# Performance work log

Measured on AMD Instinct MI355X. Metric: run time of the kernel, lower is better.

## Reference

```python
import jax, jax.numpy as jnp
import numpy as np

D = 1024
H = 16
HD = D // H
SCALE = HD ** -0.5
EPS = 1e-5

def _ln(x, g, b):
    m = jnp.mean(x, axis=-1, keepdims=True)
    v = jnp.mean((x - m) ** 2, axis=-1, keepdims=True)
    return (x - m) / jnp.sqrt(v + EPS) * g + b

def setup_inputs() -> dict:
    key = jax.random.key(0)
    ks = jax.random.split(key, 16)
    B, Lq, Lk = 8, 1024, 1024
    s = 0.02
    inp = {
        "q": jax.random.normal(ks[0], (B, Lq, D), jnp.float32),
        "kv": jax.random.normal(ks[1], (B, Lk, D), jnp.float32),
        "kv_mask": jax.random.randint(ks[2], (B, Lk), 0, 2).astype(bool),
        "Wq": jax.random.normal(ks[3], (D, D), jnp.float32) * s,
        "bq": jnp.zeros((D,), jnp.float32),
        "Wk": jax.random.normal(ks[4], (D, D), jnp.float32) * s,
        "bk": jnp.zeros((D,), jnp.float32),
        "Wv": jax.random.normal(ks[5], (D, D), jnp.float32) * s,
        "bv": jnp.zeros((D,), jnp.float32),
        "Wo": jax.random.normal(ks[6], (D, D), jnp.float32) * s,
        "bo": jnp.zeros((D,), jnp.float32),
        "ln1_g": jnp.ones((D,), jnp.float32),
        "ln1_b": jnp.zeros((D,), jnp.float32),
        "W1": jax.random.normal(ks[7], (D, 4 * D), jnp.float32) * s,
        "b1": jnp.zeros((4 * D,), jnp.float32),
        "W2": jax.random.normal(ks[8], (4 * D, D), jnp.float32) * s,
        "b2": jnp.zeros((D,), jnp.float32),
        "ln2_g": jnp.ones((D,), jnp.float32),
        "ln2_b": jnp.zeros((D,), jnp.float32),
    }
    return inp

def reference(q, kv, kv_mask, Wq, bq, Wk, bk, Wv, bv, Wo, bo, ln1_g, ln1_b, W1, b1, W2, b2, ln2_g, ln2_b):
    B, Lq, _ = q.shape
    Lk = kv.shape[1]
    # projections -> [B, H, L, HD]
    qp = (q @ Wq + bq).reshape(B, Lq, H, HD).transpose(0, 2, 1, 3)
    kp = (kv @ Wk + bk).reshape(B, Lk, H, HD).transpose(0, 2, 1, 3)
    vp = (kv @ Wv + bv).reshape(B, Lk, H, HD).transpose(0, 2, 1, 3)
    scores = jnp.einsum('bhqd,bhkd->bhqk', qp, kp) * SCALE
    # mask: True = pad; if a row is all-pad, un-mask the last key position
    all_pad = jnp.all(kv_mask, axis=1)  # [B]
    mask = kv_mask.at[:, -1].set(jnp.where(all_pad, False, kv_mask[:, -1]))
    scores = jnp.where(mask[:, None, None, :], jnp.float32(-10000.0), scores)
    attn = jax.nn.softmax(scores, axis=-1)  # dropout is identity at eval
    out = jnp.einsum('bhqk,bhkd->bhqd', attn, vp)
    out = out.transpose(0, 2, 1, 3).reshape(B, Lq, D)
    out = out @ Wo + bo
    x = _ln(q + out, ln1_g, ln1_b)
    x2 = jax.nn.relu(x @ W1 + b1) @ W2 + b2
    return _ln(x + x2, ln2_g, ln2_b)
```

## Files before the change

kernel.cpp:

```cpp
#include <hip/hip_runtime.h>

typedef __bf16 bf16_t;
typedef bf16_t bf16x8 __attribute__((ext_vector_type(8)));
typedef bf16_t bf16x4 __attribute__((ext_vector_type(4)));
typedef float f32x4 __attribute__((ext_vector_type(4)));
typedef unsigned int u32;

typedef __attribute__((address_space(1))) unsigned as1_u32;
typedef __attribute__((address_space(3))) unsigned as3_u32;

#define LOG2E 1.4426950408889634f
#define QSCALE (0.125f * LOG2E)
#define MASK2 (-10000.0f * LOG2E)

__device__ __forceinline__ void gload16(const void* g, void* l) {
  __builtin_amdgcn_global_load_lds((as1_u32*)(void*)g, (as3_u32*)l, 16, 0, 0);
}

__global__ void cvt_qkv(const float* __restrict__ q, const float* __restrict__ kv,
                        bf16_t* __restrict__ qb, bf16_t* __restrict__ kvb) {
  long i = ((long)blockIdx.x * 256 + threadIdx.x) * 8;
  const float* src; bf16_t* dst;
  if (i < 8388608) { src = q + i; dst = qb + i; }
  else { src = kv + (i - 8388608); dst = kvb + (i - 8388608); }
  const float4 a = *(const float4*)src;
  const float4 b = *(const float4*)(src + 4);
  bf16x8 o;
  o[0] = (bf16_t)a.x; o[1] = (bf16_t)a.y; o[2] = (bf16_t)a.z; o[3] = (bf16_t)a.w;
  o[4] = (bf16_t)b.x; o[5] = (bf16_t)b.y; o[6] = (bf16_t)b.z; o[7] = (bf16_t)b.w;
  *(bf16x8*)dst = o;
}

__global__ void prep_mask(const unsigned char* __restrict__ mraw,
                          float* __restrict__ maskf) {
  __shared__ int sred[256];
  const int t = threadIdx.x, b = blockIdx.x;
  int f = 0;
  for (int i = t; i < 2048; i += 256) {
    u32 v = ((const u32*)mraw)[i];
    if (v & 0xFFFFFF00u) f = 1;
  }
  sred[t] = f; __syncthreads();
  for (int s = 128; s; s >>= 1) { if (t < s) sred[t] |= sred[t + s]; __syncthreads(); }
  const int isByte = sred[0];
  __syncthreads();

  int vals[4]; int allpad = 1;
#pragma unroll
  for (int i = 0; i < 4; i++) {
    int k = t * 4 + i;
    int mv = isByte ? (int)mraw[b * 1024 + k] : ((const int*)mraw)[b * 1024 + k];
    vals[i] = (mv != 0);
    allpad &= vals[i];
  }
  sred[t] = allpad; __syncthreads();
  for (int s = 128; s; s >>= 1) { if (t < s) sred[t] &= sred[t + s]; __syncthreads(); }
  const int ap = sred[0];
#pragma unroll
  for (int i = 0; i < 4; i++) {
    int k = t * 4 + i;
    int m = vals[i];
    if (ap && k == 1023) m = 0;
    maskf[b * 1024 + k] = m ? MASK2 : 0.0f;
  }
}

struct TP { const float* s; bf16_t* d; int K; int N; };
struct TP6 { TP t[6]; };
__global__ void transpose_all(TP6 args) {
  __shared__ float tile[64][65];
  int bid = blockIdx.x, z, tx, ty;
  if (bid < 1024)      { z = bid >> 8;  int r = bid & 255;  tx = r & 15; ty = r >> 4; }
  else if (bid < 2048) { z = 4;         int r = bid - 1024; tx = r & 63; ty = r >> 6; }
  else                 { z = 5;         int r = bid - 2048; tx = r & 15; ty = r >> 4; }
  const TP a = args.t[z];
  const int t = threadIdx.x;
  const int n0 = tx * 64, k0 = ty * 64;
#pragma unroll
  for (int i = 0; i < 16; i++) {
    int e = i * 256 + t; int r = e >> 6, c = e & 63;
    tile[r][c] = a.s[(size_t)(k0 + r) * a.N + n0 + c];
  }
  __syncthreads();
#pragma unroll
  for (int i = 0; i < 16; i++) {
    int e = i * 256 + t; int r = e >> 6, c = e & 63;
    a.d[(size_t)(n0 + r) * a.K + k0 + c] = (bf16_t)tile[c][r];
  }
}

template<int BM, int BN, int NT>
__global__ __launch_bounds__(NT, 2)
void gemm_bt(const bf16_t* __restrict__ A, const bf16_t* __restrict__ BT,
             const float* __restrict__ bias, bf16_t* __restrict__ C,
             int M, int N, int K, int relu, int bias_mode, float scale) {
  constexpr int WAVES = NT / 64;
  constexpr int WNC = (BN == 256) ? 4 : 2;
  constexpr int WMC = WAVES / WNC;
  constexpr int M_REP = BM / (WMC * 16);
  constexpr int N_REP = BN / (WNC * 16);
  constexpr int JA = BM * 8 / NT;
  constexpr int JB = BN * 8 / NT;

  __shared__ __align__(16) bf16_t As[2][BM * 64];
  __shared__ __align__(16) bf16_t Bs[2][BN * 64];

  const int tid = threadIdx.x;
  const int wave = tid >> 6, lane = tid & 63;
  const int quad = lane >> 4, l15 = lane & 15;
  const int gx = gridDim.x;
  const int nwg = gx * gridDim.y;
  int lin = blockIdx.y * gx + blockIdx.x;
  lin = (lin & 7) * (nwg >> 3) + (lin >> 3);
  const long bm = (long)(lin / gx) * BM, bn = (long)(lin % gx) * BN;
  const int wm = (wave / WNC) * (M_REP * 16), wn = (wave % WNC) * (N_REP * 16);

  const bf16_t* agp[JA];
  const bf16_t* bgp[JB];
#pragma unroll
  for (int j = 0; j < JA; j++) {
    int e = j * NT + tid, r = e >> 3, c = (e & 7) ^ (r & 7);
    agp[j] = A + (bm + r) * (long)K + c * 8;
  }
#pragma unroll
  for (int j = 0; j < JB; j++) {
    int e = j * NT + tid, r = e >> 3, c = (e & 7) ^ (r & 7);
    bgp[j] = BT + (bn + r) * (long)K + c * 8;
  }

  int aoff[M_REP][2], boff[N_REP][2];
#pragma unroll
  for (int mi = 0; mi < M_REP; mi++)
#pragma unroll
    for (int ks = 0; ks < 2; ks++) {
      int row = wm + mi * 16 + l15;
      aoff[mi][ks] = row * 64 + (((ks * 4 + quad) ^ (row & 7)) * 8);
    }
#pragma unroll
  for (int ni = 0; ni < N_REP; ni++)
#pragma unroll
    for (int ks = 0; ks < 2; ks++) {
      int row = wn + ni * 16 + l15;
      boff[ni][ks] = row * 64 + (((ks * 4 + quad) ^ (row & 7)) * 8);
    }

  f32x4 acc[M_REP][N_REP];
#pragma unroll
  for (int i = 0; i < M_REP; i++)
#pragma unroll
    for (int j = 0; j < N_REP; j++) acc[i][j] = (f32x4){0.f, 0.f, 0.f, 0.f};

  auto stage = [&](int kt, int s) {
#pragma unroll
    for (int j = 0; j < JA; j++)
      gload16(agp[j] + (long)kt * 64, &As[s][(j * NT + wave * 64) * 8]);
#pragma unroll
    for (int j = 0; j < JB; j++)
      gload16(bgp[j] + (long)kt * 64, &Bs[s][(j * NT + wave * 64) * 8]);
  };

  const int T = K >> 6;
  stage(0, 0);
  for (int t = 0; t < T; t++) {
    const int s = t & 1;
    if (t + 1 < T) {
      stage(t + 1, s ^ 1);
      asm volatile("s_waitcnt vmcnt(8)" ::: "memory");
    } else {
      asm volatile("s_waitcnt vmcnt(0)" ::: "memory");
    }
    __builtin_amdgcn_s_barrier();

#pragma unroll
    for (int ks = 0; ks < 2; ks++) {
      bf16x8 af[M_REP], bf[N_REP];
#pragma unroll
      for (int mi = 0; mi < M_REP; mi++) af[mi] = *(const bf16x8*)&As[s][aoff[mi][ks]];
#pragma unroll
      for (int ni = 0; ni < N_REP; ni++) bf[ni] = *(const bf16x8*)&Bs[s][boff[ni][ks]];
      __builtin_amdgcn_s_setprio(1);
#pragma unroll
      for (int mi = 0; mi < M_REP; mi++)
#pragma unroll
        for (int ni = 0; ni < N_REP; ni++)
          acc[mi][ni] = __builtin_amdgcn_mfma_f32_16x16x32_bf16(af[mi], bf[ni], acc[mi][ni], 0, 0, 0);
      __builtin_amdgcn_s_setprio(0);
    }
    asm volatile("s_waitcnt lgkmcnt(0)" ::: "memory");
    __builtin_amdgcn_s_barrier();
  }

#pragma unroll
  for (int mi = 0; mi < M_REP; mi++) {
#pragma unroll
    for (int ni = 0; ni < N_REP; ni++) {
      const long col = bn + wn + ni * 16 + l15;
      const float bc = bias_mode ? 0.f : bias[col];
#pragma unroll
      for (int r = 0; r < 4; r++) {
        const long row = bm + wm + mi * 16 + quad * 4 + r;
        const float bb = bias_mode ? bias[row] : bc;
        float v = (acc[mi][ni][r] + bb) * scale;
        if (relu) v = v > 0.f ? v : 0.f;
        C[row * N + col] = (bf16_t)v;
      }
    }
  }
}

__global__ __launch_bounds__(512, 2)
void gemm_8p(const bf16_t* __restrict__ A, const bf16_t* __restrict__ BT,
             const float* __restrict__ bias, bf16_t* __restrict__ C,
             int M, int N, int K, int relu, float scale) {
  __shared__ __align__(16) bf16_t As[2][256 * 64];
  __shared__ __align__(16) bf16_t Bs[2][256 * 64];

  const int tid = threadIdx.x;
  const int wave = tid >> 6, lane = tid & 63;
  const int quad = lane >> 4, l15 = lane & 15;
  const int gx = gridDim.x;
  const int nwg = gx * gridDim.y;
  int lin = blockIdx.y * gx + blockIdx.x;
  lin = (lin & 7) * (nwg >> 3) + (lin >> 3);
  const long bm = (long)(lin / gx) * 256, bn = (long)(lin % gx) * 256;
  const int wm = (wave >> 2) * 128, wn = (wave & 3) * 64;

  const int r_ = tid >> 3;
  const int cs_ = ((tid & 7) ^ (r_ & 7)) * 8;
  const bf16_t* ag = A + (bm + r_) * (long)K + cs_;
  const bf16_t* bg = BT + (bn + r_) * (long)K + cs_;

  int aoff[8][2], boff[4][2];
#pragma unroll
  for (int mi = 0; mi < 8; mi++)
#pragma unroll
    for (int ks = 0; ks < 2; ks++) {
      int row = wm + mi * 16 + l15;
      aoff[mi][ks] = row * 64 + (((ks * 4 + quad) ^ (row & 7)) * 8);
    }
#pragma unroll
  for (int ni = 0; ni < 4; ni++)
#pragma unroll
    for (int ks = 0; ks < 2; ks++) {
      int row = wn + ni * 16 + l15;
      boff[ni][ks] = row * 64 + (((ks * 4 + quad) ^ (row & 7)) * 8);
    }

  f32x4 acc[8][4];
#pragma unroll
  for (int i = 0; i < 8; i++)
#pragma unroll
    for (int j = 0; j < 4; j++) acc[i][j] = (f32x4){0.f, 0.f, 0.f, 0.f};

  auto stagePair = [&](int kt, int s, int j) {
    gload16(ag + (long)(j * 64) * K + (long)kt * 64, &As[s][(j * 512 + wave * 64) * 8]);
    gload16(bg + (long)(j * 64) * K + (long)kt * 64, &Bs[s][(j * 512 + wave * 64) * 8]);
  };

  const int T = K >> 6;
#pragma unroll
  for (int j = 0; j < 4; j++) stagePair(0, 0, j);

#pragma unroll 1
  for (int t = 0; t < T; t++) {
    const int s = t & 1;
    if (t + 1 < T) {
      stagePair(t + 1, s ^ 1, 0);
      asm volatile("s_waitcnt vmcnt(2)" ::: "memory");
    } else {
      asm volatile("s_waitcnt vmcnt(0)" ::: "memory");
    }
    __builtin_amdgcn_s_barrier();

    bf16x8 bf[4][2];
#pragma unroll
    for (int ni = 0; ni < 4; ni++)
#pragma unroll
      for (int ks = 0; ks < 2; ks++)
        bf[ni][ks] = *(const bf16x8*)&Bs[s][boff[ni][ks]];

#pragma unroll
    for (int p = 0; p < 4; p++) {
      bf16x8 af[2][2];
#pragma unroll
      for (int i = 0; i < 2; i++)
#pragma unroll
        for (int ks = 0; ks < 2; ks++)
          af[i][ks] = *(const bf16x8*)&As[s][aoff[p * 2 + i][ks]];
      if (p < 3 && t + 1 < T) stagePair(t + 1, s ^ 1, p + 1);
      __builtin_amdgcn_s_barrier();
      __builtin_amdgcn_s_setprio(1);
#pragma unroll
      for (int i = 0; i < 2; i++)
#pragma unroll
        for (int ni = 0; ni < 4; ni++)
#pragma unroll
          for (int ks = 0; ks < 2; ks++)
            acc[p * 2 + i][ni] = __builtin_amdgcn_mfma_f32_16x16x32_bf16(
                af[i][ks], bf[ni][ks], acc[p * 2 + i][ni], 0, 0, 0);
      __builtin_amdgcn_s_setprio(0);
      __builtin_amdgcn_s_barrier();
    }
  }

#pragma unroll
  for (int mi = 0; mi < 8; mi++) {
#pragma unroll
    for (int ni = 0; ni < 4; ni++) {
      const long col = bn + wn + ni * 16 + l15;
      const float bc = bias[col];
#pragma unroll
      for (int r = 0; r < 4; r++) {
        const long row = bm + wm + mi * 16 + quad * 4 + r;
        float v = (acc[mi][ni][r] + bc) * scale;
        if (relu) v = v > 0.f ? v : 0.f;
        C[row * N + col] = (bf16_t)v;
      }
    }
  }
}

__global__ __launch_bounds__(256, 4)
void attn(const bf16_t* __restrict__ Q, const bf16_t* __restrict__ Kp,
          const bf16_t* __restrict__ Vt, const float* __restrict__ maskf,
          bf16_t* __restrict__ AO) {
  __shared__ __align__(16) bf16_t Qs[64 * 64];
  __shared__ __align__(16) bf16_t Ks[64 * 64];
  __shared__ __align__(16) bf16_t Vts[64 * 64];
  __shared__ __align__(16) bf16_t Ps[4][16 * 64];
  __shared__ __align__(16) float msk[64];

  const int tid = threadIdx.x;
  const int wave = tid >> 6, lane = tid & 63;
  const int quad = lane >> 4, l15 = lane & 15;
  int lin = (blockIdx.z * 16 + blockIdx.y) * 16 + blockIdx.x;
  lin = (lin & 7) * 256 + (lin >> 3);
  const int q0 = (lin & 15) * 64;
  const int h = (lin >> 4) & 15;
  const int b = lin >> 8;

  const long base_q = ((long)b * 1024 + q0) * 1024 + h * 64;
  const long base_k = (long)b * 1024 * 1024 + h * 64;
  const long base_v = (long)h * 64 * 8192 + b * 1024;

  const int r0 = tid >> 3;
  const int c0 = ((tid & 7) ^ (r0 & 7)) * 8;
  const int r1 = (256 + tid) >> 3;
  const int c1 = (((256 + tid) & 7) ^ (r1 & 7)) * 8;
  const int wd0 = wave * 64 * 8;
  const int wd1 = (256 + wave * 64) * 8;

  const bf16_t* qg0 = Q + base_q + (long)r0 * 1024 + c0;
  const bf16_t* qg1 = Q + base_q + (long)r1 * 1024 + c1;
  const bf16_t* kg0 = Kp + base_k + (long)r0 * 1024 + c0;
  const bf16_t* kg1 = Kp + base_k + (long)r1 * 1024 + c1;
  const bf16_t* vg0 = Vt + base_v + (long)r0 * 8192 + c0;
  const bf16_t* vg1 = Vt + base_v + (long)r1 * 8192 + c1;
  const float* mrow = maskf + b * 1024;

  gload16(qg0, &Qs[wd0]);
  gload16(qg1, &Qs[wd1]);

  int offKV[4][2], offP[2], pwOff[4];
#pragma unroll
  for (int nt = 0; nt < 4; nt++)
#pragma unroll
    for (int ks = 0; ks < 2; ks++)
      offKV[nt][ks] = (nt * 16 + l15) * 64 + (((ks * 4 + quad) ^ (l15 & 7)) * 8);
#pragma unroll
  for (int ks = 0; ks < 2; ks++)
    offP[ks] = l15 * 64 + (((ks * 4 + quad) ^ (l15 & 7)) * 8);
#pragma unroll
  for (int nt = 0; nt < 4; nt++)
    pwOff[nt] = l15 * 64 + (((nt * 2 + (quad >> 1)) ^ (l15 & 7)) * 8) + (quad & 1) * 4;

  __syncthreads();

  bf16x8 aq[2];
#pragma unroll
  for (int ks = 0; ks < 2; ks++) {
    const int row = wave * 16 + l15;
    aq[ks] = *(const bf16x8*)&Qs[row * 64 + (((ks * 4 + quad) ^ (row & 7)) * 8)];
  }

  float l_i = 0.f;
  f32x4 o[4];
#pragma unroll
  for (int nt = 0; nt < 4; nt++) o[nt] = (f32x4){0.f, 0.f, 0.f, 0.f};

  bf16_t* Pw = &Ps[wave][0];

  for (int kt = 0; kt < 16; kt++) {
    const int k0 = kt * 64;
    __syncthreads();
    gload16(kg0 + (long)k0 * 1024, &Ks[wd0]);
    gload16(kg1 + (long)k0 * 1024, &Ks[wd1]);
    gload16(vg0 + k0, &Vts[wd0]);
    gload16(vg1 + k0, &Vts[wd1]);
    if (tid < 64) msk[tid] = mrow[k0 + tid];
    __syncthreads();

    f32x4 mv[4];
#pragma unroll
    for (int nt = 0; nt < 4; nt++)
      mv[nt] = *(const f32x4*)&msk[nt * 16 + quad * 4];

    f32x4 sc[4];
#pragma unroll
    for (int nt = 0; nt < 4; nt++) {
      f32x4 s = mv[nt];
#pragma unroll
      for (int ks = 0; ks < 2; ks++) {
        bf16x8 bk = *(const bf16x8*)&Ks[offKV[nt][ks]];
        s = __builtin_amdgcn_mfma_f32_16x16x32_bf16(bk, aq[ks], s, 0, 0, 0);
      }
      sc[nt] = s;
    }

#pragma unroll
    for (int nt = 0; nt < 4; nt++)
#pragma unroll
      for (int r = 0; r < 4; r++) {
        const float p = exp2f(sc[nt][r]);
        sc[nt][r] = p;
        l_i += p;
      }

#pragma unroll
    for (int nt = 0; nt < 4; nt++) {
      bf16x4 pv;
#pragma unroll
      for (int r = 0; r < 4; r++) pv[r] = (bf16_t)sc[nt][r];
      *(bf16x4*)&Pw[pwOff[nt]] = pv;
    }

#pragma unroll
    for (int ks = 0; ks < 2; ks++) {
      bf16x8 ap = *(const bf16x8*)&Pw[offP[ks]];
#pragma unroll
      for (int nt = 0; nt < 4; nt++) {
        bf16x8 bv = *(const bf16x8*)&Vts[offKV[nt][ks]];
        o[nt] = __builtin_amdgcn_mfma_f32_16x16x32_bf16(ap, bv, o[nt], 0, 0, 0);
      }
    }
  }

  l_i += __shfl_xor(l_i, 16);
  l_i += __shfl_xor(l_i, 32);
  float linv[4];
#pragma unroll
  for (int r = 0; r < 4; r++)
    linv[r] = 1.0f / __shfl(l_i, (quad << 4) | (quad * 4 + r));
#pragma unroll
  for (int r = 0; r < 4; r++) {
    const int row = q0 + wave * 16 + quad * 4 + r;
#pragma unroll
    for (int nt = 0; nt < 4; nt++) {
      const int col = h * 64 + nt * 16 + l15;
      AO[((long)b * 1024 + row) * 1024 + col] = (bf16_t)(o[nt][r] * linv[r]);
    }
  }
}

__global__ __launch_bounds__(256)
void ln_res1(const float* __restrict__ xa, const bf16_t* __restrict__ xb,
             const float* __restrict__ g, const float* __restrict__ bt,
             bf16_t* __restrict__ out) {
  __shared__ float sw[8];
  const int t = threadIdx.x, w = t >> 6;
  const long row = blockIdx.x;
  const float4 a = *(const float4*)(xa + row * 1024 + t * 4);
  const bf16x4 bq = *(const bf16x4*)(xb + row * 1024 + t * 4);
  float v[4] = {a.x + (float)bq[0], a.y + (float)bq[1],
                a.z + (float)bq[2], a.w + (float)bq[3]};
  float s = v[0] + v[1] + v[2] + v[3];
  float s2 = v[0]*v[0] + v[1]*v[1] + v[2]*v[2] + v[3]*v[3];
#pragma unroll
  for (int off = 1; off < 64; off <<= 1) {
    s += __shfl_xor(s, off); s2 += __shfl_xor(s2, off);
  }
  if ((t & 63) == 0) { sw[w] = s; sw[4 + w] = s2; }
  __syncthreads();
  s = sw[0] + sw[1] + sw[2] + sw[3];
  s2 = sw[4] + sw[5] + sw[6] + sw[7];
  const float mean = s * (1.f / 1024.f);
  const float var = s2 * (1.f / 1024.f) - mean * mean;
  const float rstd = rsqrtf(var + 1e-5f);
  bf16x4 o;
#pragma unroll
  for (int i = 0; i < 4; i++) {
    const int c = t * 4 + i;
    o[i] = (bf16_t)((v[i] - mean) * rstd * g[c] + bt[c]);
  }
  *(bf16x4*)(out + row * 1024 + t * 4) = o;
}

__global__ __launch_bounds__(256)
void ln_res2(const bf16_t* __restrict__ xa, const bf16_t* __restrict__ xb,
             const float* __restrict__ g, const float* __restrict__ bt,
             float* __restrict__ out) {
  __shared__ float sw[8];
  const int t = threadIdx.x, w = t >> 6;
  const long row = blockIdx.x;
  const bf16x4 aq = *(const bf16x4*)(xa + row * 1024 + t * 4);
  const bf16x4 bq = *(const bf16x4*)(xb + row * 1024 + t * 4);
  float v[4];
#pragma unroll
  for (int i = 0; i < 4; i++) v[i] = (float)aq[i] + (float)bq[i];
  float s = v[0] + v[1] + v[2] + v[3];
  float s2 = v[0]*v[0] + v[1]*v[1] + v[2]*v[2] + v[3]*v[3];
#pragma unroll
  for (int off = 1; off < 64; off <<= 1) {
    s += __shfl_xor(s, off); s2 += __shfl_xor(s2, off);
  }
  if ((t & 63) == 0) { sw[w] = s; sw[4 + w] = s2; }
  __syncthreads();
  s = sw[0] + sw[1] + sw[2] + sw[3];
  s2 = sw[4] + sw[5] + sw[6] + sw[7];
  const float mean = s * (1.f / 1024.f);
  const float var = s2 * (1.f / 1024.f) - mean * mean;
  const float rstd = rsqrtf(var + 1e-5f);
  float4 o;
  o.x = (v[0] - mean) * rstd * g[t*4+0] + bt[t*4+0];
  o.y = (v[1] - mean) * rstd * g[t*4+1] + bt[t*4+1];
  o.z = (v[2] - mean) * rstd * g[t*4+2] + bt[t*4+2];
  o.w = (v[3] - mean) * rstd * g[t*4+3] + bt[t*4+3];
  *(float4*)(out + row * 1024 + t * 4) = o;
}

extern "C" void kernel_launch(void* const* d_in, const int* in_sizes, int n_in,
                              void* d_out, int out_size, void* d_ws, size_t ws_size,
                              hipStream_t stream) {
  (void)in_sizes; (void)n_in; (void)out_size; (void)ws_size;
  const float* q   = (const float*)d_in[0];
  const float* kv  = (const float*)d_in[1];
  const unsigned char* mraw = (const unsigned char*)d_in[2];
  const float* Wq = (const float*)d_in[3];
  const float* bq = (const float*)d_in[4];
  const float* Wk = (const float*)d_in[5];
  const float* bk = (const float*)d_in[6];
  const float* Wv = (const float*)d_in[7];
  const float* bv = (const float*)d_in[8];
  const float* Wo = (const float*)d_in[9];
  const float* bo = (const float*)d_in[10];
  const float* g1 = (const float*)d_in[11];
  const float* be1 = (const float*)d_in[12];
  const float* W1 = (const float*)d_in[13];
  const float* b1 = (const float*)d_in[14];
  const float* W2 = (const float*)d_in[15];
  const float* b2 = (const float*)d_in[16];
  const float* g2 = (const float*)d_in[17];
  const float* be2 = (const float*)d_in[18];
  float* out = (float*)d_out;

  char* ws = (char*)d_ws;
  size_t off = 0;
  auto alloc = [&](size_t bytes) -> char* {
    char* p = ws + off; off += (bytes + 255) & ~(size_t)255; return p;
  };
  const size_t MB16 = (size_t)8192 * 1024 * 2;
  float*  maskf = (float*)alloc(8192 * 4);
  bf16_t* WqT = (bf16_t*)alloc((size_t)1024 * 1024 * 2);
  bf16_t* WkT = (bf16_t*)alloc((size_t)1024 * 1024 * 2);
  bf16_t* WvT = (bf16_t*)alloc((size_t)1024 * 1024 * 2);
  bf16_t* WoT = (bf16_t*)alloc((size_t)1024 * 1024 * 2);
  bf16_t* W1T = (bf16_t*)alloc((size_t)1024 * 4096 * 2);
  bf16_t* W2T = (bf16_t*)alloc((size_t)4096 * 1024 * 2);
  bf16_t* Qp = (bf16_t*)alloc(MB16);
  bf16_t* Kp = (bf16_t*)alloc(MB16);
  bf16_t* VT = (bf16_t*)alloc(MB16);
  bf16_t* AO = (bf16_t*)alloc(MB16);
  bf16_t* X1 = (bf16_t*)alloc(MB16);
  bf16_t* TL = (bf16_t*)alloc(MB16);
  bf16_t* qb  = X1;
  bf16_t* kvb = TL;
  bf16_t* HF  = Qp;
  bf16_t* OP  = Kp;
  bf16_t* F2  = WqT;

  cvt_qkv<<<8192, 256, 0, stream>>>(q, kv, qb, kvb);
  prep_mask<<<8, 256, 0, stream>>>(mraw, maskf);
  TP6 tp = {{ {Wq, WqT, 1024, 1024}, {Wk, WkT, 1024, 1024},
              {Wv, WvT, 1024, 1024}, {Wo, WoT, 1024, 1024},
              {W1, W1T, 1024, 4096}, {W2, W2T, 4096, 1024} }};
  transpose_all<<<3072, 256, 0, stream>>>(tp);

  const dim3 gproj(8, 64);
  gemm_bt<128,128,256><<<gproj, 256, 0, stream>>>(qb,  WqT, bq, Qp, 8192, 1024, 1024, 0, 0, QSCALE);
  gemm_bt<128,128,256><<<gproj, 256, 0, stream>>>(kvb, WkT, bk, Kp, 8192, 1024, 1024, 0, 0, 1.f);
  gemm_bt<128,128,256><<<dim3(64, 8), 256, 0, stream>>>(WvT, kvb, bv, VT, 1024, 8192, 1024, 0, 1, 1.f);

  attn<<<dim3(16, 16, 8), 256, 0, stream>>>(Qp, Kp, VT, maskf, AO);

  gemm_bt<128,128,256><<<gproj, 256, 0, stream>>>(AO, WoT, bo, OP, 8192, 1024, 1024, 0, 0, 1.f);
  ln_res1<<<8192, 256, 0, stream>>>(q, OP, g1, be1, X1);

  gemm_8p<<<dim3(16, 32), 512, 0, stream>>>(X1, W1T, b1, HF, 8192, 4096, 1024, 1, 1.f);
  gemm_bt<128,128,256><<<gproj, 256, 0, stream>>>(HF, W2T, b2, F2, 8192, 1024, 4096, 0, 0, 1.f);
  ln_res2<<<8192, 256, 0, stream>>>(X1, F2, g2, be2, out);
}
```

Baseline: 525.4 us.

## Reorder A-tile staging in 8-wave GEMM for finer-grained per-phase waits

Changes the A-tile LDS layout in the 256x256 GEMM so each of the four compute phases reads a contiguous 64-row slot covering both wave groups. B is prefetched first and A in quarter chunks, with a staggered vmcnt wait before each phase. This lets compute on early phases begin before the whole next tile has landed, and it drops one barrier per phase. The cost is more complex wait-count logic that must exactly match the load order.

```diff
diff --git a/kernel.cpp b/kernel.cpp
--- a/kernel.cpp
+++ b/kernel.cpp
@@ -218,26 +218,30 @@
   const int tid = threadIdx.x;
   const int wave = tid >> 6, lane = tid & 63;
   const int quad = lane >> 4, l15 = lane & 15;
+  const int g = wave >> 2;
+  const int wn = (wave & 3) * 64;
   const int gx = gridDim.x;
   const int nwg = gx * gridDim.y;
   int lin = blockIdx.y * gx + blockIdx.x;
   lin = (lin & 7) * (nwg >> 3) + (lin >> 3);
   const long bm = (long)(lin / gx) * 256, bn = (long)(lin % gx) * 256;
-  const int wm = (wave >> 2) * 128, wn = (wave & 3) * 64;
 
   const int r_ = tid >> 3;
   const int cs_ = ((tid & 7) ^ (r_ & 7)) * 8;
-  const bf16_t* ag = A + (bm + r_) * (long)K + cs_;
+  const int arow = r_ + ((r_ >= 32) ? 96 : 0);
+  const bf16_t* ag = A + (bm + arow) * (long)K + cs_;
   const bf16_t* bg = BT + (bn + r_) * (long)K + cs_;
 
-  int aoff[8][2], boff[4][2];
-#pragma unroll
-  for (int mi = 0; mi < 8; mi++)
-#pragma unroll
-    for (int ks = 0; ks < 2; ks++) {
-      int row = wm + mi * 16 + l15;
-      aoff[mi][ks] = row * 64 + (((ks * 4 + quad) ^ (row & 7)) * 8);
-    }
+  int aoff[4][2][2], boff[4][2];
+#pragma unroll
+  for (int p = 0; p < 4; p++)
+#pragma unroll
+    for (int i = 0; i < 2; i++)
+#pragma unroll
+      for (int ks = 0; ks < 2; ks++) {
+        int slot = p * 64 + g * 32 + i * 16 + l15;
+        aoff[p][i][ks] = slot * 64 + (((ks * 4 + quad) ^ (l15 & 7)) * 8);
+      }
 #pragma unroll
   for (int ni = 0; ni < 4; ni++)
 #pragma unroll
@@ -252,43 +256,57 @@
 #pragma unroll
     for (int j = 0; j < 4; j++) acc[i][j] = (f32x4){0.f, 0.f, 0.f, 0.f};
 
-  auto stagePair = [&](int kt, int s, int j) {
-    gload16(ag + (long)(j * 64) * K + (long)kt * 64, &As[s][(j * 512 + wave * 64) * 8]);
+  auto stageB = [&](int kt, int s, int j) {
     gload16(bg + (long)(j * 64) * K + (long)kt * 64, &Bs[s][(j * 512 + wave * 64) * 8]);
   };
+  auto stageA = [&](int kt, int s, int p) {
+    gload16(ag + (long)(p * 32) * K + (long)kt * 64, &As[s][(p * 512 + wave * 64) * 8]);
+  };
 
   const int T = K >> 6;
 #pragma unroll
-  for (int j = 0; j < 4; j++) stagePair(0, 0, j);
+  for (int j = 0; j < 4; j++) stageB(0, 0, j);
+#pragma unroll
+  for (int p = 0; p < 4; p++) stageA(0, 0, p);
 
 #pragma unroll 1
   for (int t = 0; t < T; t++) {
     const int s = t & 1;
-    if (t + 1 < T) {
-      stagePair(t + 1, s ^ 1, 0);
-      asm volatile("s_waitcnt vmcnt(2)" ::: "memory");
-    } else {
-      asm volatile("s_waitcnt vmcnt(0)" ::: "memory");
-    }
-    __builtin_amdgcn_s_barrier();
+    const bool pf = (t + 1 < T);
 
     bf16x8 bf[4][2];
 #pragma unroll
-    for (int ni = 0; ni < 4; ni++)
-#pragma unroll
-      for (int ks = 0; ks < 2; ks++)
-        bf[ni][ks] = *(const bf16x8*)&Bs[s][boff[ni][ks]];
-
-#pragma unroll
     for (int p = 0; p < 4; p++) {
+      if (p == 0)      { asm volatile("s_waitcnt vmcnt(3)" ::: "memory"); }
+      else if (p == 1) { if (pf) asm volatile("s_waitcnt vmcnt(4)" ::: "memory");
+                         else    asm volatile("s_waitcnt vmcnt(2)" ::: "memory"); }
+      else if (p == 2) { if (pf) asm volatile("s_waitcnt vmcnt(5)" ::: "memory");
+                         else    asm volatile("s_waitcnt vmcnt(1)" ::: "memory"); }
+      else             { if (pf) asm volatile("s_waitcnt vmcnt(6)" ::: "memory");
+                         else    asm volatile("s_waitcnt vmcnt(0)" ::: "memory"); }
+      __builtin_amdgcn_s_barrier();
+
+      if (p == 0) {
+#pragma unroll
+        for (int ni = 0; ni < 4; ni++)
+#pragma unroll
+          for (int ks = 0; ks < 2; ks++)
+            bf[ni][ks] = *(const bf16x8*)&Bs[s][boff[ni][ks]];
+      }
       bf16x8 af[2][2];
 #pragma unroll
       for (int i = 0; i < 2; i++)
 #pragma unroll
         for (int ks = 0; ks < 2; ks++)
-          af[i][ks] = *(const bf16x8*)&As[s][aoff[p * 2 + i][ks]];
-      if (p < 3 && t + 1 < T) stagePair(t + 1, s ^ 1, p + 1);
-      __builtin_amdgcn_s_barrier();
+          af[i][ks] = *(const bf16x8*)&As[s][aoff[p][i][ks]];
+
+      if (pf) {
+        if (p == 0)      { stageB(t + 1, s ^ 1, 0); stageB(t + 1, s ^ 1, 1); }
+        else if (p == 1) { stageB(t + 1, s ^ 1, 2); stageB(t + 1, s ^ 1, 3); }
+        else if (p == 2) { stageA(t + 1, s ^ 1, 0); stageA(t + 1, s ^ 1, 1); }
+        else             { stageA(t + 1, s ^ 1, 2); stageA(t + 1, s ^ 1, 3); }
+      }
+
       __builtin_amdgcn_s_setprio(1);
 #pragma unroll
       for (int i = 0; i < 2; i++)
@@ -299,7 +317,6 @@
             acc[p * 2 + i][ni] = __builtin_amdgcn_mfma_f32_16x16x32_bf16(
                 af[i][ks], bf[ni][ks], acc[p * 2 + i][ni], 0, 0, 0);
       __builtin_amdgcn_s_setprio(0);
-      __builtin_amdgcn_s_barrier();
     }
   }
 
@@ -311,7 +328,7 @@
       const float bc = bias[col];
 #pragma unroll
       for (int r = 0; r < 4; r++) {
-        const long row = bm + wm + mi * 16 + quad * 4 + r;
+        const long row = bm + g * 128 + mi * 16 + quad * 4 + r;
         float v = (acc[mi][ni][r] + bc) * scale;
         if (relu) v = v > 0.f ? v : 0.f;
         C[row * N + col] = (bf16_t)v;
```

Result: faster. 514.0 us (-2.2%).
